# Performance work log

Hardware: AMD Instinct MI355X
Metric: run time of the kernel (lower is better)

Reference implementation:

```python
import jax, jax.numpy as jnp
import numpy as np

N_HEAD = 16
EPS = 1e-6

def setup_inputs() -> dict:
    key = jax.random.key(0)
    ks = jax.random.split(key, 5)
    B, S, D = 2, 2048, 1024
    scale = 0.02
    return {
        "hidden_states": jax.random.normal(ks[0], (B, S, D), dtype=jnp.float32),
        "w_q": jax.random.normal(ks[1], (D, D), dtype=jnp.float32) * scale,
        "w_k": jax.random.normal(ks[2], (D, D), dtype=jnp.float32) * scale,
        "w_v": jax.random.normal(ks[3], (D, D), dtype=jnp.float32) * scale,
        "w_o": jax.random.normal(ks[4], (D, D), dtype=jnp.float32) * scale,
        "qk_norm_factor": jnp.float32(1.0 / np.sqrt(D // N_HEAD)),
    }

def reference(hidden_states, w_q, w_k, w_v, w_o, qk_norm_factor):
    B, S, D = hidden_states.shape
    H = N_HEAD
    hd = D // H
    # projections (torch Linear without bias: x @ W^T)
    q = jnp.einsum('bsd,ed->bse', hidden_states, w_q).reshape(B, S, H, hd).transpose(0, 2, 1, 3)
    k = jnp.einsum('bsd,ed->bse', hidden_states, w_k).reshape(B, S, H, hd).transpose(0, 2, 1, 3)
    v = jnp.einsum('bsd,ed->bse', hidden_states, w_v).reshape(B, S, H, hd).transpose(0, 2, 1, 3)
    # hypersphere (QK) normalization
    q = q / (jnp.linalg.norm(q, axis=-1, keepdims=True) + EPS)
    k = k / (jnp.linalg.norm(k, axis=-1, keepdims=True) + EPS)
    # scores [B,H,S,S], learned scale
    scores = jnp.einsum('bhqd,bhkd->bhqk', q, k) * qk_norm_factor
    causal = jnp.tril(jnp.ones((S, S), dtype=bool))
    scores = jnp.where(causal[None, None], scores, jnp.float32(-jnp.inf))
    probs = jax.nn.softmax(scores, axis=-1)
    attn = jnp.einsum('bhqk,bhkd->bhqd', probs, v)
    attn = attn.transpose(0, 2, 1, 3).reshape(B, S, D)
    out = jnp.einsum('bsd,ed->bse', attn, w_o)
    return out
```

## Files before the change

### kernel.cpp

```cpp
#include <hip/hip_runtime.h>
#include <hip/hip_bf16.h>

typedef __attribute__((ext_vector_type(8))) short short8;
typedef __attribute__((ext_vector_type(4))) short short4v;
typedef __attribute__((ext_vector_type(4))) float floatx4;

union BF8 { short8 v; __hip_bfloat16 b[8]; };
union BF4U { ushort4 u; __hip_bfloat16 b[4]; };
union S4U { uint2 u; short4v v; };

__device__ __forceinline__ short8 load8(const __hip_bfloat16* p) {
    return *reinterpret_cast<const short8*>(p);
}
__device__ __forceinline__ short4v load4(const __hip_bfloat16* p) {
    return *reinterpret_cast<const short4v*>(p);
}

__device__ __forceinline__ void storeC(float* p, float v) { *p = v; }
__device__ __forceinline__ void storeC(__hip_bfloat16* p, float v) { *p = __float2bfloat16(v); }

__device__ __forceinline__ unsigned pack_bf16(float a, float b) {
    unsigned ua = __float_as_uint(a) + 0x8000u;
    unsigned ub = __float_as_uint(b) + 0x8000u;
    return __builtin_amdgcn_perm(ub, ua, 0x07060302u);
}

__device__ __forceinline__ float exp2_fast(float x) {
#if __has_builtin(__builtin_amdgcn_exp2f)
    return __builtin_amdgcn_exp2f(x);
#else
    return __expf(x * 0.6931471805599453f);
#endif
}

#if __has_builtin(__builtin_amdgcn_mfma_f32_16x16x16_bf16)
__device__ __forceinline__ floatx4 mfma16(short4v a, short4v b, floatx4 c) {
    return __builtin_amdgcn_mfma_f32_16x16x16_bf16(a, b, c, 0, 0, 0);
}
#elif __has_builtin(__builtin_amdgcn_mfma_f32_16x16x16bf16_1k)
__device__ __forceinline__ floatx4 mfma16(short4v a, short4v b, floatx4 c) {
    return __builtin_amdgcn_mfma_f32_16x16x16bf16_1k(a, b, c, 0, 0, 0);
}
#else
__device__ __forceinline__ floatx4 mfma16(short4v a, short4v b, floatx4 c) {
    asm volatile("v_mfma_f32_16x16x16_bf16 %0, %1, %2, %0"
                 : "+v"(c) : "v"(a), "v"(b));
    return c;
}
#endif

__device__ __forceinline__ void gload_lds16(const __hip_bfloat16* g, __hip_bfloat16* l) {
    __builtin_amdgcn_global_load_lds(
        (const __attribute__((address_space(1))) void*)g,
        (__attribute__((address_space(3))) void*)l, 16, 0, 0);
}

__global__ __launch_bounds__(256) void cast_all(const float* __restrict__ hs,
                                                const float* __restrict__ wq,
                                                const float* __restrict__ wk,
                                                const float* __restrict__ wv,
                                                const float* __restrict__ wo,
                                                __hip_bfloat16* __restrict__ Xb,
                                                __hip_bfloat16* __restrict__ Wb) {
    int i = blockIdx.x * 256 + threadIdx.x;
    const float* src;
    __hip_bfloat16* dst;
    if (blockIdx.y == 0) {
        src = hs; dst = Xb;
    } else {
        int m = i >> 18;
        src = (m == 0) ? wq : (m == 1) ? wk : (m == 2) ? wv : wo;
        src -= (size_t)m * 1048576;
        dst = Wb;
    }
    float4 v = reinterpret_cast<const float4*>(src)[i];
    BF4U u;
    u.b[0] = __float2bfloat16(v.x);
    u.b[1] = __float2bfloat16(v.y);
    u.b[2] = __float2bfloat16(v.z);
    u.b[3] = __float2bfloat16(v.w);
    reinterpret_cast<ushort4*>(dst)[i] = u.u;
}

__global__ __launch_bounds__(256) void gemm_qkv(const __hip_bfloat16* __restrict__ Xb,
                                                const __hip_bfloat16* __restrict__ Wqkv,
                                                __hip_bfloat16* __restrict__ Qb,
                                                __hip_bfloat16* __restrict__ Kb,
                                                __hip_bfloat16* __restrict__ Vt,
                                                const float* __restrict__ scale_p) {
    __shared__ __hip_bfloat16 lA[128 * 32];
    __shared__ __hip_bfloat16 lB[128 * 32];
    const int z = blockIdx.z;
    const __hip_bfloat16* A;
    const __hip_bfloat16* B;
    int m0, n0;
    if (z < 2) {
        A = Xb;
        B = Wqkv + (size_t)z * 1048576;
        m0 = blockIdx.x * 128;
        n0 = blockIdx.y * 128;
    } else {
        A = Wqkv + (size_t)2 * 1048576;
        B = Xb;
        m0 = (blockIdx.x & 7) * 128;
        n0 = (((blockIdx.x >> 3) * 8) + blockIdx.y) * 128;
    }
    const int Kd = 1024;
    const int t = threadIdx.x;
    const int w = t >> 6, l = t & 63;
    const int wr = (w >> 1) * 64, wc = (w & 1) * 64;
    const int lr = l & 15, lq = l >> 4;

    const floatx4 zero4 = {0.f, 0.f, 0.f, 0.f};
    floatx4 acc[4][4];
#pragma unroll
    for (int mt = 0; mt < 4; ++mt)
#pragma unroll
        for (int nt = 0; nt < 4; ++nt) acc[mt][nt] = zero4;

    for (int k0 = 0; k0 < Kd; k0 += 32) {
#pragma unroll
        for (int i = 0; i < 2; ++i) {
            int flat = t + i * 256;
            int row = flat >> 2, ch = flat & 3;
            gload_lds16(A + (size_t)(m0 + row) * Kd + k0 + ch * 8, lA + flat * 8);
            gload_lds16(B + (size_t)(n0 + row) * Kd + k0 + ch * 8, lB + flat * 8);
        }
        __syncthreads();
        short8 af[4], bfr[4];
#pragma unroll
        for (int mt = 0; mt < 4; ++mt)
            af[mt] = load8(lA + (wr + mt * 16 + lr) * 32 + lq * 8);
#pragma unroll
        for (int nt = 0; nt < 4; ++nt)
            bfr[nt] = load8(lB + (wc + nt * 16 + lr) * 32 + lq * 8);
#pragma unroll
        for (int mt = 0; mt < 4; ++mt)
#pragma unroll
            for (int nt = 0; nt < 4; ++nt)
                acc[mt][nt] = __builtin_amdgcn_mfma_f32_16x16x32_bf16(
                    af[mt], bfr[nt], acc[mt][nt], 0, 0, 0);
        __syncthreads();
    }

    if (z < 2) {
        const float fac = (z == 0) ? (*scale_p * 1.44269504f) : 1.0f;
#pragma unroll
        for (int mt = 0; mt < 4; ++mt)
#pragma unroll
            for (int r = 0; r < 4; ++r) {
                float ss = 0.f;
#pragma unroll
                for (int nt = 0; nt < 4; ++nt) {
                    float v = acc[mt][nt][r];
                    ss += v * v;
                }
                ss += __shfl_xor(ss, 1, 64);
                ss += __shfl_xor(ss, 2, 64);
                ss += __shfl_xor(ss, 4, 64);
                ss += __shfl_xor(ss, 8, 64);
                float inv = fac / (sqrtf(ss) + 1e-6f);
#pragma unroll
                for (int nt = 0; nt < 4; ++nt) acc[mt][nt][r] *= inv;
            }
        __hip_bfloat16* C = (z == 0) ? Qb : Kb;
#pragma unroll
        for (int mt = 0; mt < 4; ++mt)
#pragma unroll
            for (int nt = 0; nt < 4; ++nt)
#pragma unroll
                for (int r = 0; r < 4; ++r) {
                    int row = m0 + wr + mt * 16 + lq * 4 + r;
                    int col = n0 + wc + nt * 16 + lr;
                    C[(size_t)row * 1024 + col] = __float2bfloat16(acc[mt][nt][r]);
                }
    } else {
#pragma unroll
        for (int mt = 0; mt < 4; ++mt)
#pragma unroll
            for (int nt = 0; nt < 4; ++nt)
#pragma unroll
                for (int r = 0; r < 4; ++r) {
                    int e = m0 + wr + mt * 16 + lq * 4 + r;
                    int col = n0 + wc + nt * 16 + lr;
                    int bb = col >> 11, s = col & 2047;
                    Vt[(size_t)bb * 2097152 + (size_t)e * 2048 + s] =
                        __float2bfloat16(acc[mt][nt][r]);
                }
    }
}

template <typename OutT>
__global__ __launch_bounds__(256) void gemm_bt(const __hip_bfloat16* __restrict__ A,
                                               const __hip_bfloat16* __restrict__ B,
                                               OutT* __restrict__ C,
                                               int N, int Kd) {
    __shared__ __hip_bfloat16 lA[128 * 32];
    __shared__ __hip_bfloat16 lB[128 * 32];
    const int t = threadIdx.x;
    const int m0 = blockIdx.x * 128, n0 = blockIdx.y * 128;
    const int w = t >> 6, l = t & 63;
    const int wr = (w >> 1) * 64, wc = (w & 1) * 64;
    const int lr = l & 15, lq = l >> 4;

    const floatx4 zero4 = {0.f, 0.f, 0.f, 0.f};
    floatx4 acc[4][4];
#pragma unroll
    for (int mt = 0; mt < 4; ++mt)
#pragma unroll
        for (int nt = 0; nt < 4; ++nt) acc[mt][nt] = zero4;

    for (int k0 = 0; k0 < Kd; k0 += 32) {
#pragma unroll
        for (int i = 0; i < 2; ++i) {
            int flat = t + i * 256;
            int row = flat >> 2, ch = flat & 3;
            gload_lds16(A + (size_t)(m0 + row) * Kd + k0 + ch * 8, lA + flat * 8);
            gload_lds16(B + (size_t)(n0 + row) * Kd + k0 + ch * 8, lB + flat * 8);
        }
        __syncthreads();
        short8 af[4], bfr[4];
#pragma unroll
        for (int mt = 0; mt < 4; ++mt)
            af[mt] = load8(lA + (wr + mt * 16 + lr) * 32 + lq * 8);
#pragma unroll
        for (int nt = 0; nt < 4; ++nt)
            bfr[nt] = load8(lB + (wc + nt * 16 + lr) * 32 + lq * 8);
#pragma unroll
        for (int mt = 0; mt < 4; ++mt)
#pragma unroll
            for (int nt = 0; nt < 4; ++nt)
                acc[mt][nt] = __builtin_amdgcn_mfma_f32_16x16x32_bf16(
                    af[mt], bfr[nt], acc[mt][nt], 0, 0, 0);
        __syncthreads();
    }
#pragma unroll
    for (int mt = 0; mt < 4; ++mt)
#pragma unroll
        for (int nt = 0; nt < 4; ++nt)
#pragma unroll
            for (int r = 0; r < 4; ++r) {
                int row = m0 + wr + mt * 16 + lq * 4 + r;
                int col = n0 + wc + nt * 16 + lr;
                storeC(C + (size_t)row * N + col, acc[mt][nt][r]);
            }
}

__global__ __launch_bounds__(256, 2) void flash_attn(const __hip_bfloat16* __restrict__ Q,
                                                     const __hip_bfloat16* __restrict__ K,
                                                     const __hip_bfloat16* __restrict__ Vt,
                                                     __hip_bfloat16* __restrict__ O) {
    const int S = 2048, D = 1024;
    __shared__ __align__(16) char smem[65536];
    const int t = threadIdx.x;
    const int w = t >> 6, l = t & 63;
    const int lr = l & 15, lq = l >> 4;
    const int id = blockIdx.x;
    const int bh = (id & 7) * 4 + ((id >> 3) & 3);
    const int pr = id >> 5;
    const int b = bh >> 4, h = bh & 15;
    const __hip_bfloat16* Qb = Q + ((size_t)b * S) * D + h * 64;
    const __hip_bfloat16* Kb = K + ((size_t)b * S) * D + h * 64;
    const __hip_bfloat16* Vb = Vt + (size_t)bh * 64 * S;
    __hip_bfloat16* wbase = reinterpret_cast<__hip_bfloat16*>(smem) + w * 8192;
    float* buf = reinterpret_cast<float*>(smem);

    const int kr = l >> 3, ksg = (l & 7) ^ (kr & 7);
    const int vr = l >> 2, vsg = (l & 3) ^ (vr & 3);

#pragma unroll 1
    for (int tile = 0; tile < 2; ++tile) {
        const int jq = (tile == 0) ? (31 - pr) : pr;
        const int q0 = jq * 64;

        short8 bq[4][2];
#pragma unroll
        for (int nt = 0; nt < 4; ++nt)
#pragma unroll
            for (int kt = 0; kt < 2; ++kt)
                bq[nt][kt] = load8(Qb + (size_t)(q0 + nt * 16 + lr) * D + kt * 32 + lq * 8);

        const floatx4 zero4 = {0.f, 0.f, 0.f, 0.f};
        floatx4 oacc[4][4];
        float lsum[4] = {0.f, 0.f, 0.f, 0.f};
#pragma unroll
        for (int mt = 0; mt < 4; ++mt)
#pragma unroll
            for (int nt = 0; nt < 4; ++nt) oacc[mt][nt] = zero4;

        const int klast = 2 * jq + 1;
        const int kmask = 2 * jq;

        if (w <= klast) {
            {
                const int k0 = w * 32;
#pragma unroll
                for (int i = 0; i < 4; ++i)
                    gload_lds16(Kb + (size_t)(k0 + i * 8 + kr) * D + ksg * 8,
                                wbase + i * 512 + l * 8);
#pragma unroll
                for (int i = 0; i < 4; ++i)
                    gload_lds16(Vb + (size_t)(i * 16 + vr) * S + k0 + vsg * 8,
                                wbase + 4096 + i * 512 + l * 8);
            }
            int p = 0;
#pragma unroll 1
            for (int ks = w; ks <= klast; ks += 4) {
                const int k0 = ks * 32;
                asm volatile("s_waitcnt vmcnt(0)" ::: "memory");
                const __hip_bfloat16* kb = wbase + p * 2048;
                const __hip_bfloat16* vb = wbase + 4096 + p * 2048;
                short8 bk[2][2];
#pragma unroll
                for (int mt = 0; mt < 2; ++mt)
#pragma unroll
                    for (int kt = 0; kt < 2; ++kt) {
                        const int rl = mt * 16 + lr;
                        const int sg = (kt * 4 + lq) ^ (rl & 7);
                        bk[mt][kt] = load8(kb + rl * 64 + sg * 8);
                    }
                short4v bv[2][4];
#pragma unroll
                for (int mt = 0; mt < 2; ++mt)
#pragma unroll
                    for (int ntd = 0; ntd < 4; ++ntd) {
                        const int rl = ntd * 16 + lr;
                        const int sg = (mt * 2 + (lq >> 1)) ^ (rl & 3);
                        bv[mt][ntd] = load4(vb + rl * 32 + sg * 8 + (lq & 1) * 4);
                    }
                if (ks + 4 <= klast) {
                    const int kn = (ks + 4) * 32;
                    __hip_bfloat16* nb = wbase + (p ^ 1) * 2048;
#pragma unroll
                    for (int i = 0; i < 4; ++i)
                        gload_lds16(Kb + (size_t)(kn + i * 8 + kr) * D + ksg * 8,
                                    nb + i * 512 + l * 8);
#pragma unroll
                    for (int i = 0; i < 4; ++i)
                        gload_lds16(Vb + (size_t)(i * 16 + vr) * S + kn + vsg * 8,
                                    nb + 4096 + i * 512 + l * 8);
                }
                floatx4 sacc[2][4];
#pragma unroll
                for (int mt = 0; mt < 2; ++mt)
#pragma unroll
                    for (int nt = 0; nt < 4; ++nt) sacc[mt][nt] = zero4;
#pragma unroll
                for (int mt = 0; mt < 2; ++mt)
#pragma unroll
                    for (int nt = 0; nt < 4; ++nt)
#pragma unroll
                        for (int kt = 0; kt < 2; ++kt)
                            sacc[mt][nt] = __builtin_amdgcn_mfma_f32_16x16x32_bf16(
                                bk[mt][kt], bq[nt][kt], sacc[mt][nt], 0, 0, 0);
                const bool domask = ks >= kmask;
                short4v ap[2][4];
#pragma unroll
                for (int mt = 0; mt < 2; ++mt)
#pragma unroll
                    for (int nt = 0; nt < 4; ++nt) {
                        float p0 = exp2_fast(sacc[mt][nt][0]);
                        float p1 = exp2_fast(sacc[mt][nt][1]);
                        float p2 = exp2_fast(sacc[mt][nt][2]);
                        float p3 = exp2_fast(sacc[mt][nt][3]);
                        if (domask) {
                            const int qg = q0 + nt * 16 + lr;
                            const int kb2 = k0 + mt * 16 + lq * 4;
                            p0 = (kb2 + 0 <= qg) ? p0 : 0.f;
                            p1 = (kb2 + 1 <= qg) ? p1 : 0.f;
                            p2 = (kb2 + 2 <= qg) ? p2 : 0.f;
                            p3 = (kb2 + 3 <= qg) ? p3 : 0.f;
                        }
                        lsum[nt] += (p0 + p1) + (p2 + p3);
                        S4U u;
                        u.u.x = pack_bf16(p0, p1);
                        u.u.y = pack_bf16(p2, p3);
                        ap[mt][nt] = u.v;
                    }
#pragma unroll
                for (int mt = 0; mt < 2; ++mt)
#pragma unroll
                    for (int ntq = 0; ntq < 4; ++ntq)
#pragma unroll
                        for (int ntd = 0; ntd < 4; ++ntd)
                            oacc[ntq][ntd] = mfma16(ap[mt][ntq], bv[mt][ntd], oacc[ntq][ntd]);
                p ^= 1;
            }
        }

#pragma unroll
        for (int nt = 0; nt < 4; ++nt) {
            float s = lsum[nt];
            s += __shfl_xor(s, 16, 64);
            s += __shfl_xor(s, 32, 64);
            lsum[nt] = s;
        }

        const int row = t >> 2, c0 = (t & 3) * 4;
        __hip_bfloat16* Ob = O + ((size_t)b * S) * D + h * 64;
        float inv = 0.f;
        __syncthreads();
#pragma unroll
        for (int chunk = 0; chunk < 4; ++chunk) {
#pragma unroll
            for (int mtq = 0; mtq < 4; ++mtq)
#pragma unroll
                for (int r = 0; r < 4; ++r)
                    buf[w * 1280 + (mtq * 16 + lq * 4 + r) * 20 + lr] = oacc[mtq][chunk][r];
            if (chunk == 0 && lq == 0) {
#pragma unroll
                for (int nt = 0; nt < 4; ++nt)
                    buf[w * 1280 + (nt * 16 + lr) * 20 + 16] = lsum[nt];
            }
            __syncthreads();
            if (chunk == 0) {
                float Lt = buf[row * 20 + 16] + buf[1280 + row * 20 + 16] +
                           buf[2560 + row * 20 + 16] + buf[3840 + row * 20 + 16];
                inv = 1.f / Lt;
            }
            float4 a = {0.f, 0.f, 0.f, 0.f};
#pragma unroll
            for (int w2 = 0; w2 < 4; ++w2) {
                float4 v = *reinterpret_cast<const float4*>(buf + w2 * 1280 + row * 20 + c0);
                a.x += v.x; a.y += v.y; a.z += v.z; a.w += v.w;
            }
            uint2 d;
            d.x = pack_bf16(a.x * inv, a.y * inv);
            d.y = pack_bf16(a.z * inv, a.w * inv);
            *reinterpret_cast<uint2*>(Ob + (size_t)(q0 + row) * D + chunk * 16 + c0) = d;
            if (chunk < 3) __syncthreads();
        }
    }
}

extern "C" void kernel_launch(void* const* d_in, const int* in_sizes, int n_in,
                              void* d_out, int out_size, void* d_ws, size_t ws_size,
                              hipStream_t stream) {
    const float* hs  = (const float*)d_in[0];
    const float* wq  = (const float*)d_in[1];
    const float* wk  = (const float*)d_in[2];
    const float* wv  = (const float*)d_in[3];
    const float* wo  = (const float*)d_in[4];
    const float* qkf = (const float*)d_in[5];

    char* ws = (char*)d_ws;
    const size_t MB = 1024 * 1024;
    __hip_bfloat16* Xb  = (__hip_bfloat16*)(ws);
    __hip_bfloat16* Wqb = (__hip_bfloat16*)(ws + 8 * MB);
    __hip_bfloat16* Wob = (__hip_bfloat16*)(ws + 14 * MB);
    __hip_bfloat16* Qb  = (__hip_bfloat16*)(ws + 16 * MB);
    __hip_bfloat16* Kb  = (__hip_bfloat16*)(ws + 24 * MB);
    __hip_bfloat16* Vt  = (__hip_bfloat16*)(ws + 40 * MB);
    __hip_bfloat16* Ab  = (__hip_bfloat16*)(ws + 48 * MB);

    cast_all<<<dim3(4096, 2), 256, 0, stream>>>(hs, wq, wk, wv, wo, Xb, Wqb);

    gemm_qkv<<<dim3(32, 8, 3), 256, 0, stream>>>(Xb, Wqb, Qb, Kb, Vt, qkf);

    flash_attn<<<512, 256, 0, stream>>>(Qb, Kb, Vt, Ab);

    gemm_bt<float><<<dim3(32, 8), 256, 0, stream>>>(Ab, Wob, (float*)d_out, 1024, 1024);
}
```

Baseline: 180.7 us.

## Share K/V tiles across waves in flash attention and shrink output GEMM tile

Flash attention previously had each wave independently stream its own 32-key K/V chunks with private double buffers. It now loads one shared 128-key K/V supertile per block into LDS, synchronized with barriers. Q is also staged through LDS with a swizzled layout, and LDS drops from 64KB to 32KB with the occupancy hint removed. The output projection GEMM uses 64x128 tiles to launch twice as many blocks. The trade-off is that per-wave prefetch overlap is lost to block-wide barriers with no double buffering, and fully masked keys in the last supertile may be computed.

Result: slower. 200.1 us (+10.7%).

```diff
diff --git a/kernel.cpp b/kernel.cpp
--- a/kernel.cpp
+++ b/kernel.cpp
@@ -15,9 +15,6 @@
 __device__ __forceinline__ short4v load4(const __hip_bfloat16* p) {
     return *reinterpret_cast<const short4v*>(p);
 }
-
-__device__ __forceinline__ void storeC(float* p, float v) { *p = v; }
-__device__ __forceinline__ void storeC(__hip_bfloat16* p, float v) { *p = __float2bfloat16(v); }
 
 __device__ __forceinline__ unsigned pack_bf16(float a, float b) {
     unsigned ua = __float_as_uint(a) + 0x8000u;
@@ -190,44 +187,43 @@
     }
 }
 
-template <typename OutT>
-__global__ __launch_bounds__(256) void gemm_bt(const __hip_bfloat16* __restrict__ A,
-                                               const __hip_bfloat16* __restrict__ B,
-                                               OutT* __restrict__ C,
-                                               int N, int Kd) {
-    __shared__ __hip_bfloat16 lA[128 * 32];
+__global__ __launch_bounds__(256) void gemm_out(const __hip_bfloat16* __restrict__ A,
+                                                const __hip_bfloat16* __restrict__ B,
+                                                float* __restrict__ C) {
+    __shared__ __hip_bfloat16 lA[64 * 32];
     __shared__ __hip_bfloat16 lB[128 * 32];
+    const int Kd = 1024, N = 1024;
     const int t = threadIdx.x;
-    const int m0 = blockIdx.x * 128, n0 = blockIdx.y * 128;
+    const int m0 = blockIdx.x * 64, n0 = blockIdx.y * 128;
     const int w = t >> 6, l = t & 63;
-    const int wr = (w >> 1) * 64, wc = (w & 1) * 64;
+    const int wr = (w >> 1) * 32, wc = (w & 1) * 64;
     const int lr = l & 15, lq = l >> 4;
 
     const floatx4 zero4 = {0.f, 0.f, 0.f, 0.f};
-    floatx4 acc[4][4];
-#pragma unroll
-    for (int mt = 0; mt < 4; ++mt)
+    floatx4 acc[2][4];
+#pragma unroll
+    for (int mt = 0; mt < 2; ++mt)
 #pragma unroll
         for (int nt = 0; nt < 4; ++nt) acc[mt][nt] = zero4;
 
     for (int k0 = 0; k0 < Kd; k0 += 32) {
+        gload_lds16(A + (size_t)(m0 + (t >> 2)) * Kd + k0 + (t & 3) * 8, lA + t * 8);
 #pragma unroll
         for (int i = 0; i < 2; ++i) {
             int flat = t + i * 256;
-            int row = flat >> 2, ch = flat & 3;
-            gload_lds16(A + (size_t)(m0 + row) * Kd + k0 + ch * 8, lA + flat * 8);
-            gload_lds16(B + (size_t)(n0 + row) * Kd + k0 + ch * 8, lB + flat * 8);
-        }
-        __syncthreads();
-        short8 af[4], bfr[4];
-#pragma unroll
-        for (int mt = 0; mt < 4; ++mt)
+            gload_lds16(B + (size_t)(n0 + (flat >> 2)) * Kd + k0 + (flat & 3) * 8,
+                        lB + flat * 8);
+        }
+        __syncthreads();
+        short8 af[2], bfr[4];
+#pragma unroll
+        for (int mt = 0; mt < 2; ++mt)
             af[mt] = load8(lA + (wr + mt * 16 + lr) * 32 + lq * 8);
 #pragma unroll
         for (int nt = 0; nt < 4; ++nt)
             bfr[nt] = load8(lB + (wc + nt * 16 + lr) * 32 + lq * 8);
 #pragma unroll
-        for (int mt = 0; mt < 4; ++mt)
+        for (int mt = 0; mt < 2; ++mt)
 #pragma unroll
             for (int nt = 0; nt < 4; ++nt)
                 acc[mt][nt] = __builtin_amdgcn_mfma_f32_16x16x32_bf16(
@@ -235,23 +231,26 @@
         __syncthreads();
     }
 #pragma unroll
-    for (int mt = 0; mt < 4; ++mt)
+    for (int mt = 0; mt < 2; ++mt)
 #pragma unroll
         for (int nt = 0; nt < 4; ++nt)
 #pragma unroll
             for (int r = 0; r < 4; ++r) {
                 int row = m0 + wr + mt * 16 + lq * 4 + r;
                 int col = n0 + wc + nt * 16 + lr;
-                storeC(C + (size_t)row * N + col, acc[mt][nt][r]);
-            }
-}
-
-__global__ __launch_bounds__(256, 2) void flash_attn(const __hip_bfloat16* __restrict__ Q,
-                                                     const __hip_bfloat16* __restrict__ K,
-                                                     const __hip_bfloat16* __restrict__ Vt,
-                                                     __hip_bfloat16* __restrict__ O) {
+                C[(size_t)row * N + col] = acc[mt][nt][r];
+            }
+}
+
+__global__ __launch_bounds__(256) void flash_attn(const __hip_bfloat16* __restrict__ Q,
+                                                  const __hip_bfloat16* __restrict__ K,
+                                                  const __hip_bfloat16* __restrict__ Vt,
+                                                  __hip_bfloat16* __restrict__ O) {
     const int S = 2048, D = 1024;
-    __shared__ __align__(16) char smem[65536];
+    __shared__ __align__(16) char smem[32768];
+    __hip_bfloat16* kbuf = reinterpret_cast<__hip_bfloat16*>(smem);
+    __hip_bfloat16* vbuf = reinterpret_cast<__hip_bfloat16*>(smem + 16384);
+    float* buf = reinterpret_cast<float*>(smem);
     const int t = threadIdx.x;
     const int w = t >> 6, l = t & 63;
     const int lr = l & 15, lq = l >> 4;
@@ -262,23 +261,29 @@
     const __hip_bfloat16* Qb = Q + ((size_t)b * S) * D + h * 64;
     const __hip_bfloat16* Kb = K + ((size_t)b * S) * D + h * 64;
     const __hip_bfloat16* Vb = Vt + (size_t)bh * 64 * S;
-    __hip_bfloat16* wbase = reinterpret_cast<__hip_bfloat16*>(smem) + w * 8192;
-    float* buf = reinterpret_cast<float*>(smem);
-
-    const int kr = l >> 3, ksg = (l & 7) ^ (kr & 7);
-    const int vr = l >> 2, vsg = (l & 3) ^ (vr & 3);
 
 #pragma unroll 1
     for (int tile = 0; tile < 2; ++tile) {
         const int jq = (tile == 0) ? (31 - pr) : pr;
         const int q0 = jq * 64;
 
+        __syncthreads();
+#pragma unroll
+        for (int i = 0; i < 2; ++i) {
+            int flat = t + i * 256;
+            int row = flat >> 3, sg = (flat & 7) ^ (row & 7);
+            gload_lds16(Qb + (size_t)(q0 + row) * D + sg * 8, kbuf + flat * 8);
+        }
+        __syncthreads();
         short8 bq[4][2];
 #pragma unroll
         for (int nt = 0; nt < 4; ++nt)
 #pragma unroll
-            for (int kt = 0; kt < 2; ++kt)
-                bq[nt][kt] = load8(Qb + (size_t)(q0 + nt * 16 + lr) * D + kt * 32 + lq * 8);
+            for (int kt = 0; kt < 2; ++kt) {
+                const int rl = nt * 16 + lr;
+                const int sg = (kt * 4 + lq) ^ (rl & 7);
+                bq[nt][kt] = load8(kbuf + rl * 64 + sg * 8);
+            }
 
         const floatx4 zero4 = {0.f, 0.f, 0.f, 0.f};
         floatx4 oacc[4][4];
@@ -288,104 +293,91 @@
 #pragma unroll
             for (int nt = 0; nt < 4; ++nt) oacc[mt][nt] = zero4;
 
-        const int klast = 2 * jq + 1;
+        const int nss = (2 * jq + 5) >> 2;
         const int kmask = 2 * jq;
 
-        if (w <= klast) {
-            {
-                const int k0 = w * 32;
-#pragma unroll
-                for (int i = 0; i < 4; ++i)
-                    gload_lds16(Kb + (size_t)(k0 + i * 8 + kr) * D + ksg * 8,
-                                wbase + i * 512 + l * 8);
-#pragma unroll
-                for (int i = 0; i < 4; ++i)
-                    gload_lds16(Vb + (size_t)(i * 16 + vr) * S + k0 + vsg * 8,
-                                wbase + 4096 + i * 512 + l * 8);
-            }
-            int p = 0;
 #pragma unroll 1
-            for (int ks = w; ks <= klast; ks += 4) {
-                const int k0 = ks * 32;
-                asm volatile("s_waitcnt vmcnt(0)" ::: "memory");
-                const __hip_bfloat16* kb = wbase + p * 2048;
-                const __hip_bfloat16* vb = wbase + 4096 + p * 2048;
-                short8 bk[2][2];
-#pragma unroll
-                for (int mt = 0; mt < 2; ++mt)
-#pragma unroll
-                    for (int kt = 0; kt < 2; ++kt) {
-                        const int rl = mt * 16 + lr;
-                        const int sg = (kt * 4 + lq) ^ (rl & 7);
-                        bk[mt][kt] = load8(kb + rl * 64 + sg * 8);
+        for (int ss = 0; ss < nss; ++ss) {
+            const int kbase = ss * 128;
+            __syncthreads();
+#pragma unroll
+            for (int i = 0; i < 4; ++i) {
+                int flat = t + i * 256;
+                int row = flat >> 3, sg = (flat & 7) ^ (row & 7);
+                gload_lds16(Kb + (size_t)(kbase + row) * D + sg * 8, kbuf + flat * 8);
+            }
+#pragma unroll
+            for (int i = 0; i < 4; ++i) {
+                int flat = t + i * 256;
+                int row = flat >> 4, sg = (flat & 15) ^ (row & 15);
+                gload_lds16(Vb + (size_t)row * S + kbase + sg * 8, vbuf + flat * 8);
+            }
+            __syncthreads();
+
+            const int ks = ss * 4 + w;
+            const int k0 = ks * 32;
+            short8 bk[2][2];
+#pragma unroll
+            for (int mt = 0; mt < 2; ++mt)
+#pragma unroll
+                for (int kt = 0; kt < 2; ++kt) {
+                    const int rl = w * 32 + mt * 16 + lr;
+                    const int sg = (kt * 4 + lq) ^ (rl & 7);
+                    bk[mt][kt] = load8(kbuf + rl * 64 + sg * 8);
+                }
+            floatx4 sacc[2][4];
+#pragma unroll
+            for (int mt = 0; mt < 2; ++mt)
+#pragma unroll
+                for (int nt = 0; nt < 4; ++nt) sacc[mt][nt] = zero4;
+#pragma unroll
+            for (int mt = 0; mt < 2; ++mt)
+#pragma unroll
+                for (int nt = 0; nt < 4; ++nt)
+#pragma unroll
+                    for (int kt = 0; kt < 2; ++kt)
+                        sacc[mt][nt] = __builtin_amdgcn_mfma_f32_16x16x32_bf16(
+                            bk[mt][kt], bq[nt][kt], sacc[mt][nt], 0, 0, 0);
+            short4v bv[2][4];
+#pragma unroll
+            for (int mt = 0; mt < 2; ++mt)
+#pragma unroll
+                for (int ntd = 0; ntd < 4; ++ntd) {
+                    const int rl = ntd * 16 + lr;
+                    const int sg = (w * 4 + mt * 2 + (lq >> 1)) ^ (rl & 15);
+                    bv[mt][ntd] = load4(vbuf + rl * 128 + sg * 8 + (lq & 1) * 4);
+                }
+            const bool domask = ks >= kmask;
+            short4v ap[2][4];
+#pragma unroll
+            for (int mt = 0; mt < 2; ++mt)
+#pragma unroll
+                for (int nt = 0; nt < 4; ++nt) {
+                    float p0 = exp2_fast(sacc[mt][nt][0]);
+                    float p1 = exp2_fast(sacc[mt][nt][1]);
+                    float p2 = exp2_fast(sacc[mt][nt][2]);
+                    float p3 = exp2_fast(sacc[mt][nt][3]);
+                    if (domask) {
+                        const int qg = q0 + nt * 16 + lr;
+                        const int kb2 = k0 + mt * 16 + lq * 4;
+                        p0 = (kb2 + 0 <= qg) ? p0 : 0.f;
+                        p1 = (kb2 + 1 <= qg) ? p1 : 0.f;
+                        p2 = (kb2 + 2 <= qg) ? p2 : 0.f;
+                        p3 = (kb2 + 3 <= qg) ? p3 : 0.f;
                     }
-                short4v bv[2][4];
-#pragma unroll
-                for (int mt = 0; mt < 2; ++mt)
-#pragma unroll
-                    for (int ntd = 0; ntd < 4; ++ntd) {
-                        const int rl = ntd * 16 + lr;
-                        const int sg = (mt * 2 + (lq >> 1)) ^ (rl & 3);
-                        bv[mt][ntd] = load4(vb + rl * 32 + sg * 8 + (lq & 1) * 4);
-                    }
-                if (ks + 4 <= klast) {
-                    const int kn = (ks + 4) * 32;
-                    __hip_bfloat16* nb = wbase + (p ^ 1) * 2048;
-#pragma unroll
-                    for (int i = 0; i < 4; ++i)
-                        gload_lds16(Kb + (size_t)(kn + i * 8 + kr) * D + ksg * 8,
-                                    nb + i * 512 + l * 8);
-#pragma unroll
-                    for (int i = 0; i < 4; ++i)
-                        gload_lds16(Vb + (size_t)(i * 16 + vr) * S + kn + vsg * 8,
-                                    nb + 4096 + i * 512 + l * 8);
-                }
-                floatx4 sacc[2][4];
-#pragma unroll
-                for (int mt = 0; mt < 2; ++mt)
-#pragma unroll
-                    for (int nt = 0; nt < 4; ++nt) sacc[mt][nt] = zero4;
-#pragma unroll
-                for (int mt = 0; mt < 2; ++mt)
-#pragma unroll
-                    for (int nt = 0; nt < 4; ++nt)
-#pragma unroll
-                        for (int kt = 0; kt < 2; ++kt)
-                            sacc[mt][nt] = __builtin_amdgcn_mfma_f32_16x16x32_bf16(
-                                bk[mt][kt], bq[nt][kt], sacc[mt][nt], 0, 0, 0);
-                const bool domask = ks >= kmask;
-                short4v ap[2][4];
-#pragma unroll
-                for (int mt = 0; mt < 2; ++mt)
-#pragma unroll
-                    for (int nt = 0; nt < 4; ++nt) {
-                        float p0 = exp2_fast(sacc[mt][nt][0]);
-                        float p1 = exp2_fast(sacc[mt][nt][1]);
-                        float p2 = exp2_fast(sacc[mt][nt][2]);
-                        float p3 = exp2_fast(sacc[mt][nt][3]);
-                        if (domask) {
-                            const int qg = q0 + nt * 16 + lr;
-                            const int kb2 = k0 + mt * 16 + lq * 4;
-                            p0 = (kb2 + 0 <= qg) ? p0 : 0.f;
-                            p1 = (kb2 + 1 <= qg) ? p1 : 0.f;
-                            p2 = (kb2 + 2 <= qg) ? p2 : 0.f;
-                            p3 = (kb2 + 3 <= qg) ? p3 : 0.f;
-                        }
-                        lsum[nt] += (p0 + p1) + (p2 + p3);
-                        S4U u;
-                        u.u.x = pack_bf16(p0, p1);
-                        u.u.y = pack_bf16(p2, p3);
-                        ap[mt][nt] = u.v;
-                    }
-#pragma unroll
-                for (int mt = 0; mt < 2; ++mt)
-#pragma unroll
-                    for (int ntq = 0; ntq < 4; ++ntq)
-#pragma unroll
-                        for (int ntd = 0; ntd < 4; ++ntd)
-                            oacc[ntq][ntd] = mfma16(ap[mt][ntq], bv[mt][ntd], oacc[ntq][ntd]);
-                p ^= 1;
-            }
+                    lsum[nt] += (p0 + p1) + (p2 + p3);
+                    S4U u;
+                    u.u.x = pack_bf16(p0, p1);
+                    u.u.y = pack_bf16(p2, p3);
+                    ap[mt][nt] = u.v;
+                }
+#pragma unroll
+            for (int mt = 0; mt < 2; ++mt)
+#pragma unroll
+                for (int ntq = 0; ntq < 4; ++ntq)
+#pragma unroll
+                    for (int ntd = 0; ntd < 4; ++ntd)
+                        oacc[ntq][ntd] = mfma16(ap[mt][ntq], bv[mt][ntd], oacc[ntq][ntd]);
         }
 
 #pragma unroll
@@ -459,5 +451,5 @@
 
     flash_attn<<<512, 256, 0, stream>>>(Qb, Kb, Vt, Ab);
 
-    gemm_bt<float><<<dim3(32, 8), 256, 0, stream>>>(Ab, Wob, (float*)d_out, 1024, 1024);
-}
+    gemm_out<<<dim3(64, 8), 256, 0, stream>>>(Ab, Wob, (float*)d_out);
+}
```
